# Kernel tuning notes

Measured on AMD Instinct MI355X. Metric: run time of the kernel, lower is better.

Reference implementation:

```python
import jax, jax.numpy as jnp
import numpy as np

NUM_EXPERTS = 64
TOP_K = 2
NOISE_EPS = 0.01


def setup_inputs() -> dict:
    key = jax.random.key(0)
    k1, k2, k3, k4 = jax.random.split(key, 4)
    B, D, E = 32768, 2048, NUM_EXPERTS
    x = jax.random.normal(k1, (B, D), dtype=jnp.float32)
    # original inits these to zero; use small random weights for a non-degenerate top-k
    w_gate = jax.random.normal(k2, (D, E), dtype=jnp.float32) * 0.02
    w_noise = jax.random.normal(k3, (D, E), dtype=jnp.float32) * 0.02
    noise = jax.random.normal(k4, (B, E), dtype=jnp.float32)  # tf.random.normal draw, fixed
    return {"x": x, "w_gate": w_gate, "w_noise": w_noise, "noise": noise}


def reference(x, w_gate, w_noise, noise):
    # routing_pooling='flatten' on a 2D input is identity
    pooled = x  # [B, D]
    routing = pooled @ w_gate  # [B, E]
    # noisy routing (training=True path)
    noise_stddev = jax.nn.softplus(pooled @ w_noise) + NOISE_EPS
    routing = routing + noise * noise_stddev
    # softmax_top_k: take top k+1, keep top k, softmax, scatter back to E experts
    kk = min(TOP_K + 1, NUM_EXPERTS)
    top_vals, top_idx = jax.lax.top_k(routing, kk)
    top_k_vals = top_vals[:, :TOP_K]            # [B, k]
    top_k_idx = top_idx[:, :TOP_K]              # [B, k]
    top_k_gates = jax.nn.softmax(top_k_vals, axis=-1)
    B = routing.shape[0]
    rows = jnp.arange(B)[:, None]
    # rowwise_unsorted_segment_sum -> scatter gates into expert slots
    out = jnp.zeros((B, NUM_EXPERTS), dtype=routing.dtype).at[rows, top_k_idx].add(top_k_gates)
    return out
```

## Files before the change

### kernel.cpp

```cpp
#include <hip/hip_runtime.h>
#include <math.h>


typedef _Float16 half8v __attribute__((ext_vector_type(8)));
typedef float f32x16 __attribute__((ext_vector_type(16)));

constexpr int DIMK = 2048;
constexpr int NEXP = 64;
constexpr int BM   = 128;
constexpr int BK   = 64;
constexpr int NST  = DIMK / BK;

__device__ __forceinline__ void async_load16(const void* g, void* l) {
    __builtin_amdgcn_global_load_lds(
        (const __attribute__((address_space(1))) unsigned int*)g,
        (__attribute__((address_space(3))) unsigned int*)l, 16, 0, 0);
}

__device__ __forceinline__ bool gt_pair(float a, int ia, float b, int ib) {
    return (a > b) || (a == b && ia < ib);
}

__global__ __launch_bounds__(256)
void presplit_kernel(const float* __restrict__ wg, const float* __restrict__ wn,
                     _Float16* __restrict__ wsB)
{
    int gid  = blockIdx.x * 256 + threadIdx.x;
    int lane = gid & 63;
    int fb   = gid >> 6;
    int nt   = fb & 3;
    int p    = (fb >> 2) & 1;
    int kh   = (fb >> 3) & 1;
    int c    = fb >> 4;
    const float* src = (nt < 2) ? (wg + nt * 32 + (lane & 31))
                                : (wn + (nt - 2) * 32 + (lane & 31));
    int kb = c * 32 + kh * 16 + ((lane >> 5) << 3);
    half8v hp;
    #pragma unroll
    for (int j = 0; j < 8; ++j) {
        float w = src[(size_t)(kb + j) * NEXP] * 65536.0f;
        _Float16 a = (_Float16)w;
        hp[j] = p ? (_Float16)(w - (float)a) : a;
    }
    *(half8v*)(wsB + (size_t)fb * 512 + lane * 8) = hp;
}

__global__ __launch_bounds__(1024, 4)
void routing_mfma(const float* __restrict__ x, const _Float16* __restrict__ wsB,
                  const float* __restrict__ noise, float* __restrict__ out)
{
    __shared__ __align__(16) char smem[131072];
    _Float16* Bs = (_Float16*)smem;
    float*    Xs = (float*)(smem + 65536);

    const int tid  = threadIdx.x;
    const int lane = tid & 63;
    const int w    = tid >> 6;
    const int rg   = w >> 2;
    const int t    = w & 3;
    const int m    = lane & 31;
    const int h    = lane >> 5;
    const int row0 = blockIdx.x * BM;

    f32x16 acc = {};

    const int lr0 = (w * 2 + 0) * 4 + (lane >> 4);
    const int lr1 = (w * 2 + 1) * 4 + (lane >> 4);
    const int ss0 = (lane & 15) ^ (lr0 & 7);
    const int ss1 = (lane & 15) ^ (lr1 & 7);
    const float* xsrc0 = x + (size_t)(row0 + lr0) * DIMK + ss0 * 4;
    const float* xsrc1 = x + (size_t)(row0 + lr1) * DIMK + ss1 * 4;

    auto stage = [&](int s, int buf) {
        #pragma unroll
        for (int i = 0; i < 2; ++i) {
            int j = w + i * 16;
            async_load16(wsB + ((size_t)s * 32 + j) * 512 + lane * 8,
                         Bs + buf * 16384 + j * 512);
        }
        async_load16(xsrc0 + s * BK, Xs + buf * 8192 + (w * 2 + 0) * 256);
        async_load16(xsrc1 + s * BK, Xs + buf * 8192 + (w * 2 + 1) * 256);
    };

    stage(0, 0);
    stage(1, 1);
    __syncthreads();

    const int r   = rg * 32 + m;
    const int rx7 = r & 7;

    for (int s = 0; s < NST; ++s) {
        const int buf = s & 1;
        const float* xrow = Xs + buf * 8192 + r * 64;

        #pragma unroll
        for (int u = 0; u < 2; ++u) {
            const _Float16* bb = Bs + buf * 16384 + u * 8192 + t * 512 + lane * 8;

            half8v bH0 = *(const half8v*)(bb);
            half8v bL0 = *(const half8v*)(bb + 2048);
            half8v bH1 = *(const half8v*)(bb + 4096);
            half8v bL1 = *(const half8v*)(bb + 6144);

            float4 x00 = *(const float4*)(xrow + ((u * 8 + h * 2 + 0) ^ rx7) * 4);
            float4 x01 = *(const float4*)(xrow + ((u * 8 + h * 2 + 1) ^ rx7) * 4);
            float4 x10 = *(const float4*)(xrow + ((u * 8 + 4 + h * 2 + 0) ^ rx7) * 4);
            float4 x11 = *(const float4*)(xrow + ((u * 8 + 4 + h * 2 + 1) ^ rx7) * 4);

            half8v aH0, aL0, aH1, aL1;
            {
                float f[8] = {x00.x, x00.y, x00.z, x00.w, x01.x, x01.y, x01.z, x01.w};
                #pragma unroll
                for (int j = 0; j < 8; ++j) {
                    float v = f[j] * 1024.f;
                    _Float16 a = (_Float16)v;
                    aH0[j] = a; aL0[j] = (_Float16)(v - (float)a);
                }
            }
            {
                float f[8] = {x10.x, x10.y, x10.z, x10.w, x11.x, x11.y, x11.z, x11.w};
                #pragma unroll
                for (int j = 0; j < 8; ++j) {
                    float v = f[j] * 1024.f;
                    _Float16 a = (_Float16)v;
                    aH1[j] = a; aL1[j] = (_Float16)(v - (float)a);
                }
            }

            acc = __builtin_amdgcn_mfma_f32_32x32x16_f16(aH0, bH0, acc, 0, 0, 0);
            acc = __builtin_amdgcn_mfma_f32_32x32x16_f16(aH0, bL0, acc, 0, 0, 0);
            acc = __builtin_amdgcn_mfma_f32_32x32x16_f16(aL0, bH0, acc, 0, 0, 0);
            acc = __builtin_amdgcn_mfma_f32_32x32x16_f16(aH1, bH1, acc, 0, 0, 0);
            acc = __builtin_amdgcn_mfma_f32_32x32x16_f16(aH1, bL1, acc, 0, 0, 0);
            acc = __builtin_amdgcn_mfma_f32_32x32x16_f16(aL1, bH1, acc, 0, 0, 0);
        }

        __syncthreads();
        if (s + 2 < NST) stage(s + 2, buf);
    }

    const float s = 0x1p-26f;
    constexpr int SLD = 68;
    float* scr = (float*)smem;
    {
        const int pl   = (t >> 1) * BM * SLD;
        const int colb = (t & 1) * 32 + m;
        #pragma unroll
        for (int reg = 0; reg < 16; ++reg) {
            int rl = (reg & 3) + 8 * (reg >> 2) + 4 * h;
            scr[pl + (rg * 32 + rl) * SLD + colb] = acc[reg] * s;
        }
    }
    __syncthreads();

    {
        int rr = tid >> 3;
        int s8 = tid & 7;
        const float* gp = scr + rr * SLD + s8 * 8;
        const float* np = scr + BM * SLD + rr * SLD + s8 * 8;
        float4 g0 = *(const float4*)(gp);
        float4 g1 = *(const float4*)(gp + 4);
        float4 n0 = *(const float4*)(np);
        float4 n1 = *(const float4*)(np + 4);
        float4 z0 = *(const float4*)(noise + (size_t)(row0 + rr) * NEXP + s8 * 8);
        float4 z1 = *(const float4*)(noise + (size_t)(row0 + rr) * NEXP + s8 * 8 + 4);
        float gg[8] = {g0.x, g0.y, g0.z, g0.w, g1.x, g1.y, g1.z, g1.w};
        float nn[8] = {n0.x, n0.y, n0.z, n0.w, n1.x, n1.y, n1.z, n1.w};
        float zz[8] = {z0.x, z0.y, z0.z, z0.w, z1.x, z1.y, z1.z, z1.w};
        float v1 = -INFINITY, v2 = -INFINITY;
        int   i1 = 0x7ffffffe,  i2 = 0x7fffffff;
        #pragma unroll
        for (int j = 0; j < 8; ++j) {
            float nv = nn[j];
            float sp = fmaxf(nv, 0.f) + log1pf(expf(-fabsf(nv)));
            float vv = gg[j] + zz[j] * (sp + 0.01f);
            int   e  = s8 * 8 + j;
            if (gt_pair(vv, e, v1, i1)) { v2 = v1; i2 = i1; v1 = vv; i1 = e; }
            else if (gt_pair(vv, e, v2, i2)) { v2 = vv; i2 = e; }
        }
        #pragma unroll
        for (int mm = 1; mm <= 4; mm <<= 1) {
            float b1 = __shfl_xor(v1, mm); int ib1 = __shfl_xor(i1, mm);
            float b2 = __shfl_xor(v2, mm); int ib2 = __shfl_xor(i2, mm);
            if (gt_pair(b1, ib1, v1, i1)) {
                float o1 = v1; int oi1 = i1;
                v1 = b1; i1 = ib1;
                if (gt_pair(b2, ib2, o1, oi1)) { v2 = b2; i2 = ib2; }
                else                           { v2 = o1; i2 = oi1; }
            } else if (gt_pair(b1, ib1, v2, i2)) {
                v2 = b1; i2 = ib1;
            }
        }
        float te = expf(v2 - v1);
        float ga = 1.f / (1.f + te);
        float gb = te * ga;
        float* op = out + (size_t)(row0 + rr) * NEXP + s8 * 8;
        #pragma unroll
        for (int qq = 0; qq < 2; ++qq) {
            int e0 = s8 * 8 + qq * 4;
            float4 o;
            o.x = (e0 + 0 == i1) ? ga : ((e0 + 0 == i2) ? gb : 0.f);
            o.y = (e0 + 1 == i1) ? ga : ((e0 + 1 == i2) ? gb : 0.f);
            o.z = (e0 + 2 == i1) ? ga : ((e0 + 2 == i2) ? gb : 0.f);
            o.w = (e0 + 3 == i1) ? ga : ((e0 + 3 == i2) ? gb : 0.f);
            *(float4*)(op + qq * 4) = o;
        }
    }
}

extern "C" void kernel_launch(void* const* d_in, const int* in_sizes, int n_in,
                              void* d_out, int out_size, void* d_ws, size_t ws_size,
                              hipStream_t stream) {
    const float* x     = (const float*)d_in[0];
    const float* wg    = (const float*)d_in[1];
    const float* wn    = (const float*)d_in[2];
    const float* noise = (const float*)d_in[3];
    float* out = (float*)d_out;
    _Float16* wsB = (_Float16*)d_ws;

    presplit_kernel<<<dim3(256), 256, 0, stream>>>(wg, wn, wsB);

    const int Brows = in_sizes[0] / DIMK;
    dim3 grid(Brows / BM);
    routing_mfma<<<grid, 1024, 0, stream>>>(x, wsB, noise, out);
}
```

Measured before the change: 398.0 us.

## Split K across wave pairs so each A fragment feeds gate and noise MFMAs

Reassigns the 16 waves so each wave owns one 32-column slice of both gate and noise outputs and half of each K step, with two accumulators. Each A fragment is converted to hi/lo halves once and reused for both gate and noise MFMAs, halving the per-wave x LDS reads and conversion work. The X swizzle is widened to 16 slots. The cost is a second accumulator per wave and a two-phase reduction of the partial sums through LDS, with an extra barrier in the epilogue.

```diff
diff --git a/kernel.cpp b/kernel.cpp
--- a/kernel.cpp
+++ b/kernel.cpp
@@ -57,24 +57,25 @@
     const int lane = tid & 63;
     const int w    = tid >> 6;
     const int rg   = w >> 2;
-    const int t    = w & 3;
+    const int t    = (w >> 1) & 1;
+    const int ks   = w & 1;
     const int m    = lane & 31;
     const int h    = lane >> 5;
     const int row0 = blockIdx.x * BM;
 
-    f32x16 acc = {};
+    f32x16 acc0 = {}, acc1 = {};
 
     const int lr0 = (w * 2 + 0) * 4 + (lane >> 4);
     const int lr1 = (w * 2 + 1) * 4 + (lane >> 4);
-    const int ss0 = (lane & 15) ^ (lr0 & 7);
-    const int ss1 = (lane & 15) ^ (lr1 & 7);
+    const int ss0 = (lane & 15) ^ (lr0 & 15);
+    const int ss1 = (lane & 15) ^ (lr1 & 15);
     const float* xsrc0 = x + (size_t)(row0 + lr0) * DIMK + ss0 * 4;
     const float* xsrc1 = x + (size_t)(row0 + lr1) * DIMK + ss1 * 4;
 
     auto stage = [&](int s, int buf) {
         #pragma unroll
         for (int i = 0; i < 2; ++i) {
-            int j = w + i * 16;
+            int j = w * 2 + i;
             async_load16(wsB + ((size_t)s * 32 + j) * 512 + lane * 8,
                          Bs + buf * 16384 + j * 512);
         }
@@ -86,8 +87,8 @@
     stage(1, 1);
     __syncthreads();
 
-    const int r   = rg * 32 + m;
-    const int rx7 = r & 7;
+    const int r    = rg * 32 + m;
+    const int rx15 = r & 15;
 
     for (int s = 0; s < NST; ++s) {
         const int buf = s & 1;
@@ -95,63 +96,66 @@
 
         #pragma unroll
         for (int u = 0; u < 2; ++u) {
-            const _Float16* bb = Bs + buf * 16384 + u * 8192 + t * 512 + lane * 8;
-
-            half8v bH0 = *(const half8v*)(bb);
-            half8v bL0 = *(const half8v*)(bb + 2048);
-            half8v bH1 = *(const half8v*)(bb + 4096);
-            half8v bL1 = *(const half8v*)(bb + 6144);
-
-            float4 x00 = *(const float4*)(xrow + ((u * 8 + h * 2 + 0) ^ rx7) * 4);
-            float4 x01 = *(const float4*)(xrow + ((u * 8 + h * 2 + 1) ^ rx7) * 4);
-            float4 x10 = *(const float4*)(xrow + ((u * 8 + 4 + h * 2 + 0) ^ rx7) * 4);
-            float4 x11 = *(const float4*)(xrow + ((u * 8 + 4 + h * 2 + 1) ^ rx7) * 4);
-
-            half8v aH0, aL0, aH1, aL1;
+            const _Float16* bb = Bs + buf * 16384 + u * 8192
+                               + (ks * 8) * 512 + lane * 8;
+
+            half8v bH0 = *(const half8v*)(bb + (t    ) * 512);
+            half8v bH1 = *(const half8v*)(bb + (2 + t) * 512);
+            half8v bL0 = *(const half8v*)(bb + (4 + t    ) * 512);
+            half8v bL1 = *(const half8v*)(bb + (4 + 2 + t) * 512);
+
+            float4 x0 = *(const float4*)(xrow + ((u * 8 + ks * 4 + h * 2 + 0) ^ rx15) * 4);
+            float4 x1 = *(const float4*)(xrow + ((u * 8 + ks * 4 + h * 2 + 1) ^ rx15) * 4);
+
+            half8v aH, aL;
             {
-                float f[8] = {x00.x, x00.y, x00.z, x00.w, x01.x, x01.y, x01.z, x01.w};
+                float f[8] = {x0.x, x0.y, x0.z, x0.w, x1.x, x1.y, x1.z, x1.w};
                 #pragma unroll
                 for (int j = 0; j < 8; ++j) {
                     float v = f[j] * 1024.f;
                     _Float16 a = (_Float16)v;
-                    aH0[j] = a; aL0[j] = (_Float16)(v - (float)a);
+                    aH[j] = a; aL[j] = (_Float16)(v - (float)a);
                 }
             }
-            {
-                float f[8] = {x10.x, x10.y, x10.z, x10.w, x11.x, x11.y, x11.z, x11.w};
-                #pragma unroll
-                for (int j = 0; j < 8; ++j) {
-                    float v = f[j] * 1024.f;
-                    _Float16 a = (_Float16)v;
-                    aH1[j] = a; aL1[j] = (_Float16)(v - (float)a);
-                }
-            }
-
-            acc = __builtin_amdgcn_mfma_f32_32x32x16_f16(aH0, bH0, acc, 0, 0, 0);
-            acc = __builtin_amdgcn_mfma_f32_32x32x16_f16(aH0, bL0, acc, 0, 0, 0);
-            acc = __builtin_amdgcn_mfma_f32_32x32x16_f16(aL0, bH0, acc, 0, 0, 0);
-            acc = __builtin_amdgcn_mfma_f32_32x32x16_f16(aH1, bH1, acc, 0, 0, 0);
-            acc = __builtin_amdgcn_mfma_f32_32x32x16_f16(aH1, bL1, acc, 0, 0, 0);
-            acc = __builtin_amdgcn_mfma_f32_32x32x16_f16(aL1, bH1, acc, 0, 0, 0);
+
+            acc0 = __builtin_amdgcn_mfma_f32_32x32x16_f16(aH, bH0, acc0, 0, 0, 0);
+            acc0 = __builtin_amdgcn_mfma_f32_32x32x16_f16(aH, bL0, acc0, 0, 0, 0);
+            acc0 = __builtin_amdgcn_mfma_f32_32x32x16_f16(aL, bH0, acc0, 0, 0, 0);
+            acc1 = __builtin_amdgcn_mfma_f32_32x32x16_f16(aH, bH1, acc1, 0, 0, 0);
+            acc1 = __builtin_amdgcn_mfma_f32_32x32x16_f16(aH, bL1, acc1, 0, 0, 0);
+            acc1 = __builtin_amdgcn_mfma_f32_32x32x16_f16(aL, bH1, acc1, 0, 0, 0);
         }
 
         __syncthreads();
         if (s + 2 < NST) stage(s + 2, buf);
     }
 
-    const float s = 0x1p-26f;
+    const float sc = 0x1p-26f;
     constexpr int SLD = 68;
     float* scr = (float*)smem;
     {
-        const int pl   = (t >> 1) * BM * SLD;
-        const int colb = (t & 1) * 32 + m;
-        #pragma unroll
-        for (int reg = 0; reg < 16; ++reg) {
-            int rl = (reg & 3) + 8 * (reg >> 2) + 4 * h;
-            scr[pl + (rg * 32 + rl) * SLD + colb] = acc[reg] * s;
-        }
-    }
-    __syncthreads();
+        const int colb = t * 32 + m;
+        if (ks == 0) {
+            #pragma unroll
+            for (int reg = 0; reg < 16; ++reg) {
+                int rl = (reg & 3) + 8 * (reg >> 2) + 4 * h;
+                scr[(rg * 32 + rl) * SLD + colb]            = acc0[reg] * sc;
+                scr[BM * SLD + (rg * 32 + rl) * SLD + colb] = acc1[reg] * sc;
+            }
+        }
+        __syncthreads();
+        if (ks == 1) {
+            #pragma unroll
+            for (int reg = 0; reg < 16; ++reg) {
+                int rl = (reg & 3) + 8 * (reg >> 2) + 4 * h;
+                int ig = (rg * 32 + rl) * SLD + colb;
+                int in = BM * SLD + ig;
+                scr[ig] += acc0[reg] * sc;
+                scr[in] += acc1[reg] * sc;
+            }
+        }
+        __syncthreads();
+    }
 
     {
         int rr = tid >> 3;
```

Result: no change. 398.1 us (+0.0%).
